# Kernel tuning notes

Hardware: AMD Instinct MI355X
Metric: run time of the kernel (lower is better)

The kernel has to match this reference:

```python
import jax, jax.numpy as jnp
import numpy as np

B, N, K = 2, 8192, 9
IN_CH, FEAT_CH, COST_CH = 64, 128, 64

def _bn(x, p, eps=1e-5):
    # eval-mode BatchNorm; p is [4, C] = (gamma, beta, running_mean, running_var)
    sh = (1, -1) + (1,) * (x.ndim - 2)
    g, b, m, v = (p[i].reshape(sh) for i in range(4))
    return (x - m) / jnp.sqrt(v + eps) * g + b

def _c1(x, w, b):
    # Conv1d kernel 1: x [B,C,N], w [O,C]
    return jnp.einsum('oc,bcn->bon', w, x) + b[None, :, None]

def _forward(xyz, points, cost_volume, feats, flow,
             w0, b0, bn0, w1, b1, bn1,
             wz, bz, wr, br, wq, bq,
             w2a, b2a, w2b, b2b, wfc, bfc,
             rw0, rbn0, rw1, rbn1, rw2, rbn2,
             cw0, cbn0, cw1, cbn1, cw2, cbn2):
    lrelu = lambda t: jax.nn.leaky_relu(t, 0.1)
    # --- self-KNN on xyz ---
    xt = jnp.transpose(xyz, (0, 2, 1))                   # B N 3
    sq = jnp.sum(xt * xt, -1)                            # B N
    d2 = sq[:, :, None] + sq[:, None, :] - 2.0 * jnp.einsum('bnd,bmd->bnm', xt, xt)
    idx = jax.lax.top_k(-d2, K)[1]                       # B N K (nearest incl. self)
    # --- grouping_operation: gather neighbor features ---
    np0 = jnp.concatenate([cost_volume, flow], 1)        # B (cost_ch+3) N
    g = jax.vmap(lambda p, i: p[:, i])(np0, idx)         # B C N K
    # --- Conv2d(1x1)+BN+LeakyReLU stack ---
    g = lrelu(_bn(jnp.einsum('oc,bcnk->bonk', w0, g) + b0[None, :, None, None], bn0))
    g = lrelu(_bn(jnp.einsum('oc,bcnk->bonk', w1, g) + b1[None, :, None, None], bn1))
    h = jnp.max(g, -1)                                   # max over neighbors -> B 128 N
    # --- ConvGRU(x=feats, h) with 1x1 Conv1d gates ---
    hx = jnp.concatenate([h, feats], 1)
    z = jax.nn.sigmoid(_c1(hx, wz, bz))
    r = jax.nn.sigmoid(_c1(hx, wr, br))
    q = jnp.tanh(_c1(jnp.concatenate([r * h, feats], 1), wq, bq))
    h = (1.0 - z) * h + z * q
    # --- Conv1d MLP head ---
    x = jnp.concatenate([points, h], 1)                  # B (in_ch+128) N
    x = lrelu(_c1(x, w2a, b2a))
    x = lrelu(_c1(x, w2b, b2b))
    re_flow = _c1(x, wfc, bfc)                           # B 3 N
    # --- prob regnets (Conv1d no-bias + BN + ReLU) ---
    def reg(y, ws, ps):
        for w, p in zip(ws, ps):
            y = jax.nn.relu(_bn(jnp.einsum('oc,bcn->bon', w, y), p))
        return y
    refine = reg(x, [rw0, rw1, rw2], [rbn0, rbn1, rbn2])         # B 1 N
    coarse = reg(cost_volume, [cw0, cw1, cw2], [cbn0, cbn1, cbn2])
    re_flow = coarse * flow + refine * re_flow
    return x, jnp.clip(re_flow, -20.0, 20.0)

def setup_inputs():
    key = jax.random.key(0)
    ks = iter(jax.random.split(key, 80))
    nrm = lambda shape, s=1.0: jax.random.normal(next(ks), shape, jnp.float32) * s
    def bnp(C):
        g = jax.random.uniform(next(ks), (C,), jnp.float32) + 0.5
        b = nrm((C,), 0.1); m = nrm((C,), 0.1)
        v = jax.random.uniform(next(ks), (C,), jnp.float32) + 0.5
        return jnp.stack([g, b, m, v])
    z = lambda C: jnp.zeros((C,), jnp.float32)
    return dict(
        xyz=nrm((B, 3, N)), points=nrm((B, IN_CH, N)), cost_volume=nrm((B, COST_CH, N)),
        feats=nrm((B, FEAT_CH, N)), flow=nrm((B, 3, N), 0.1),
        w0=nrm((128, COST_CH + 3), 0.05), b0=z(128), bn0=bnp(128),
        w1=nrm((128, 128), 0.05), b1=z(128), bn1=bnp(128),
        wz=nrm((128, 256), 0.05), bz=z(128), wr=nrm((128, 256), 0.05), br=z(128),
        wq=nrm((128, 256), 0.05), bq=z(128),
        w2a=nrm((128, IN_CH + 128), 0.05), b2a=z(128), w2b=nrm((64, 128), 0.05), b2b=z(64),
        wfc=nrm((3, 64), 0.05), bfc=z(3),
        rw0=nrm((64, 64), 0.05), rbn0=bnp(64), rw1=nrm((64, 64), 0.05), rbn1=bnp(64),
        rw2=nrm((1, 64), 0.05), rbn2=bnp(1),
        cw0=nrm((64, COST_CH), 0.05), cbn0=bnp(64), cw1=nrm((64, 64), 0.05), cbn1=bnp(64),
        cw2=nrm((1, 64), 0.05), cbn2=bnp(1),
    )

def reference(xyz, points, cost_volume, feats, flow, w0, b0, bn0, w1, b1, bn1, wz, bz, wr, br, wq, bq, w2a, b2a, w2b, b2b, wfc, bfc, rw0, rbn0, rw1, rbn1, rw2, rbn2, cw0, cbn0, cw1, cbn1, cw2, cbn2):
    return _forward(xyz, points, cost_volume, feats, flow, w0, b0, bn0, w1, b1, bn1, wz, bz, wr, br, wq, bq, w2a, b2a, w2b, b2b, wfc, bfc, rw0, rbn0, rw1, rbn1, rw2, rbn2, cw0, cbn0, cw1, cbn1, cw2, cbn2)
```

## Files before the change

### kernel.cpp

```cpp
#include <hip/hip_runtime.h>
#include <math.h>

typedef __bf16 bf16;
typedef __bf16 bf16x8 __attribute__((ext_vector_type(8)));
typedef float f32x4 __attribute__((ext_vector_type(4)));

#define NPTS 8192
#define MTOT 16384

static __device__ __forceinline__ float b2f(bf16 x) { return (float)x; }
static __device__ __forceinline__ bf16  f2b(float x) { return (bf16)x; }

__global__ void diag_k(float* out, float code)
{
    if (threadIdx.x == 0 && blockIdx.x == 0) out[0] = code;
}

static __device__ __forceinline__ void pack_body(bf16 (*tile)[68],
                                                 const float* __restrict__ src, int Csrc,
                                                 bf16* __restrict__ dst, int ldd,
                                                 int nb, int cb, int b)
{
    const int t = threadIdx.x;
#pragma unroll
    for (int i = 0; i < 8; ++i) {
        int id = t + i * 256;
        int c = id >> 6, n = id & 63;
        int cc = cb + c;
        bf16 v = (bf16)0.0f;
        if (cc < Csrc) v = f2b(src[(size_t)(b * Csrc + cc) * NPTS + nb + n]);
        tile[c][n] = v;
    }
    __syncthreads();
#pragma unroll
    for (int i = 0; i < 8; ++i) {
        int id = t + i * 256;
        int n = id >> 5, c = id & 31;
        dst[(size_t)(b * NPTS + nb + n) * ldd + cb + c] = tile[c][n];
    }
}

static __device__ __forceinline__ float tau_decode(unsigned long long k8)
{
    unsigned u = (unsigned)(k8 >> 32);
    unsigned m = 0x80000000u | (unsigned)(~((int)u >> 31));
    return __uint_as_float(u ^ m);
}

static __device__ __forceinline__ void mm32(
    f32x4 (&acc)[2][2],
    const bf16* A1, int lda1, int row01, int K1,
    const bf16* A2, int lda2, int row02,
    const bf16* W, int ldw, int K, int ob)
{
    const int lane = threadIdx.x & 63;
    const int q = lane >> 4, r = lane & 15;
    const bf16* Wp = W + (size_t)(ob + r) * ldw + q * 8;
    for (int k = 0; k < K; k += 32) {
        const bf16* Ap; int ld;
        if (k < K1) { ld = lda1; Ap = A1 + (size_t)(row01 + r) * lda1 + q * 8 + k; }
        else        { ld = lda2; Ap = A2 + (size_t)(row02 + r) * lda2 + q * 8 + (k - K1); }
        bf16x8 bv0 = *(const bf16x8*)(Wp + k);
        bf16x8 bv1 = *(const bf16x8*)(Wp + 16 * ldw + k);
        bf16x8 a0 = *(const bf16x8*)(Ap);
        bf16x8 a1 = *(const bf16x8*)(Ap + 16 * ld);
        acc[0][0] = __builtin_amdgcn_mfma_f32_16x16x32_bf16(a0, bv0, acc[0][0], 0, 0, 0);
        acc[1][0] = __builtin_amdgcn_mfma_f32_16x16x32_bf16(a1, bv0, acc[1][0], 0, 0, 0);
        acc[0][1] = __builtin_amdgcn_mfma_f32_16x16x32_bf16(a0, bv1, acc[0][1], 0, 0, 0);
        acc[1][1] = __builtin_amdgcn_mfma_f32_16x16x32_bf16(a1, bv1, acc[1][1], 0, 0, 0);
    }
}

static __device__ __forceinline__ void zacc(f32x4 (&acc)[2][2])
{
    f32x4 z = {0.f, 0.f, 0.f, 0.f};
    acc[0][0] = z; acc[0][1] = z; acc[1][0] = z; acc[1][1] = z;
}

__global__ __launch_bounds__(256) void pack_a(
    const float* __restrict__ w0, const float* __restrict__ w1,
    const float* __restrict__ wz, const float* __restrict__ wr,
    const float* __restrict__ wq, const float* __restrict__ w2a,
    const float* __restrict__ w2b, const float* __restrict__ rw0,
    const float* __restrict__ rw1, const float* __restrict__ cw0,
    const float* __restrict__ cw1,
    const float* __restrict__ cost, const float* __restrict__ flow,
    bf16* __restrict__ w0p, bf16* __restrict__ wts,
    bf16* __restrict__ CV, bf16* __restrict__ FL)
{
    __shared__ __align__(16) bf16 tile[32][68];
    const int bx = blockIdx.x;
    if (bx < 48) {
        int id = bx * 256 + threadIdx.x;
        if (id < 128 * 96) {
            int o = id / 96, c = id - o * 96;
            w0p[id] = (c < 67) ? f2b(w0[o * 67 + c]) : (bf16)0.0f;
        }
    } else if (bx < 688) {
        int id = (bx - 48) * 256 + threadIdx.x;
        if (id < 163840) {
            const float* s; int off;
            if (id < 16384)       { s = w1;  off = 0; }
            else if (id < 49152)  { s = wz;  off = 16384; }
            else if (id < 81920)  { s = wr;  off = 49152; }
            else if (id < 114688) { s = wq;  off = 81920; }
            else if (id < 139264) { s = w2a; off = 114688; }
            else if (id < 147456) { s = w2b; off = 139264; }
            else if (id < 151552) { s = rw0; off = 147456; }
            else if (id < 155648) { s = rw1; off = 151552; }
            else if (id < 159744) { s = cw0; off = 155648; }
            else                  { s = cw1; off = 159744; }
            wts[id] = f2b(s[id - off]);
        }
    } else if (bx < 1200) {
        int l = bx - 688, x = l & 127, r2 = l >> 7;
        pack_body(tile, cost, 64, CV, 64, x * 64, (r2 & 1) * 32, r2 >> 1);
    } else {
        int l = bx - 1200, x = l & 127, b = l >> 7;
        pack_body(tile, flow, 3, FL, 32, x * 64, 0, b);
    }
}

__global__ __launch_bounds__(256, 5) void knn_conv_packb(
    const float* __restrict__ xyz, const float* __restrict__ feats,
    const float* __restrict__ points,
    const bf16* __restrict__ CV, const bf16* __restrict__ FL,
    const bf16* __restrict__ W0p, const bf16* __restrict__ W1,
    const float* __restrict__ b0, const float* __restrict__ bn0,
    const float* __restrict__ b1, const float* __restrict__ bn1,
    bf16* __restrict__ FE, bf16* __restrict__ PT,
    bf16* __restrict__ P2, int* __restrict__ idxg)
{
    __shared__ __align__(16) char smem[16384];
    const int bx = blockIdx.x;
    if (bx < 4096) {
        float4* pts = (float4*)smem;
        const int t = threadIdx.x, lane = t & 63, w = t >> 6;
        const int qid = bx * 4 + w, b = qid >> 13;
        const float* X = xyz + b * 3 * NPTS;
        const int n = qid & (NPTS - 1);
        const float qx = X[n], qy = X[NPTS + n], qz = X[2 * NPTS + n];
        const float qsq = qx * qx + qy * qy + qz * qz;

        unsigned long long kk[9];
#pragma unroll
        for (int k = 0; k < 9; ++k) kk[k] = ~0ull;
        float tau = __builtin_inff();

        for (int ch = 0; ch < 8; ++ch) {
            __syncthreads();
#pragma unroll
            for (int r2 = 0; r2 < 4; ++r2) {
                int i2 = t + r2 * 256;
                int ci = ch * 1024 + i2;
                float x = X[ci], y = X[NPTS + ci], z = X[2 * NPTS + ci];
                pts[i2] = make_float4(x, y, z, x * x + y * y + z * z);
            }
            __syncthreads();
            int i0 = 0;
            if (ch == 0) {
                float4 c = pts[lane];
                float d = (qsq + c.w) - 2.0f * (qx * c.x + qy * c.y + qz * c.z);
                unsigned kd = __float_as_uint(d);
                kd ^= ((unsigned)((int)kd >> 31)) | 0x80000000u;
                unsigned long long key = ((unsigned long long)kd << 32) | (unsigned)lane;
#pragma unroll
                for (int r = 0; r < 9; ++r) {
                    unsigned long long m = key;
#pragma unroll
                    for (int s = 1; s < 64; s <<= 1) {
                        unsigned long long o = __shfl_xor(m, s);
                        if (o < m) m = o;
                    }
                    kk[r] = m;
                    if (key == m) key = ~0ull;
                }
                tau = tau_decode(kk[8]);
                i0 = 1;
            }
            for (int i = i0; i < 16; ++i) {
                float4 c = pts[i * 64 + lane];
                float d = (qsq + c.w) - 2.0f * (qx * c.x + qy * c.y + qz * c.z);
                unsigned long long mask = __ballot(d <= tau);
                if (mask) {
                    const int base = ch * 1024 + i * 64;
                    do {
                        int L = __builtin_ctzll(mask);
                        mask &= mask - 1;
                        float dL = __uint_as_float(
                            (unsigned)__builtin_amdgcn_readlane(__float_as_int(d), L));
                        unsigned kd = __float_as_uint(dL);
                        kd ^= ((unsigned)((int)kd >> 31)) | 0x80000000u;
                        unsigned long long K = ((unsigned long long)kd << 32)
                                             | (unsigned)(base + L);
                        if (K < kk[8]) {
                            bool lt[9];
#pragma unroll
                            for (int j2 = 0; j2 < 9; ++j2) lt[j2] = K < kk[j2];
#pragma unroll
                            for (int j2 = 8; j2 > 0; --j2)
                                kk[j2] = lt[j2] ? (lt[j2 - 1] ? kk[j2 - 1] : K) : kk[j2];
                            kk[0] = lt[0] ? K : kk[0];
                            tau = tau_decode(kk[8]);
                        }
                    } while (mask);
                }
            }
        }
        if (lane == 0) {
#pragma unroll
            for (int k = 0; k < 9; ++k) {
                int m = (int)(unsigned)(kk[k] & 0xffffffffu);
                m = ((unsigned)m < (unsigned)NPTS) ? m : 0;
                idxg[qid * 9 + k] = b * NPTS + m;
            }
        }
    } else if (bx < 4608) {
        bf16 (*P1t)[136] = (bf16 (*)[136])smem;
        const int w = threadIdx.x >> 6, lane = threadIdx.x & 63;
        const int q = lane >> 4, r = lane & 15;
        const int ptb = (bx - 4096) * 32;
        {
            f32x4 acc[2][2]; zacc(acc);
            const int ob = w * 32;
            mm32(acc, CV, 64, ptb, 64, FL, 32, ptb, W0p, 96, 96, ob);
#pragma unroll
            for (int to = 0; to < 2; ++to) {
                const int o = ob + to * 16 + r;
                float bs = b0[o];
                float gg = bn0[o], be = bn0[128 + o], mm = bn0[256 + o];
                float rs = 1.0f / sqrtf(bn0[384 + o] + 1e-5f);
#pragma unroll
                for (int tm = 0; tm < 2; ++tm) {
#pragma unroll
                    for (int rr = 0; rr < 4; ++rr) {
                        const int jl = tm * 16 + q * 4 + rr;
                        float v = acc[tm][to][rr] + bs;
                        v = (v - mm) * rs * gg + be;
                        v = v > 0.f ? v : 0.1f * v;
                        P1t[jl][o] = f2b(v);
                    }
                }
            }
        }
        __syncthreads();
        {
            f32x4 acc[2][2]; zacc(acc);
            const int ob = w * 32;
            mm32(acc, &P1t[0][0], 136, 0, 128, &P1t[0][0], 136, 0, W1, 128, 128, ob);
#pragma unroll
            for (int to = 0; to < 2; ++to) {
                const int o = ob + to * 16 + r;
                float bs = b1[o];
                float gg = bn1[o], be = bn1[128 + o], mm = bn1[256 + o];
                float rs = 1.0f / sqrtf(bn1[384 + o] + 1e-5f);
#pragma unroll
                for (int tm = 0; tm < 2; ++tm) {
#pragma unroll
                    for (int rr = 0; rr < 4; ++rr) {
                        const int jl = tm * 16 + q * 4 + rr;
                        float v = acc[tm][to][rr] + bs;
                        v = (v - mm) * rs * gg + be;
                        v = v > 0.f ? v : 0.1f * v;
                        P2[(size_t)(ptb + jl) * 128 + o] = f2b(v);
                    }
                }
            }
        }
    } else if (bx < 5632) {
        bf16 (*tile)[68] = (bf16 (*)[68])smem;
        int l = bx - 4608, x = l & 127, r2 = l >> 7;
        pack_body(tile, feats, 128, FE, 128, x * 64, (r2 & 3) * 32, r2 >> 2);
    } else {
        bf16 (*tile)[68] = (bf16 (*)[68])smem;
        int l = bx - 5632, x = l & 127, r2 = l >> 7;
        pack_body(tile, points, 64, PT, 64, x * 64, (r2 & 1) * 32, r2 >> 1);
    }
}

struct MRP {
    const bf16 *P2, *FE, *PT, *CV;
    const int  *idx;
    const bf16 *WZ, *WR, *WQ, *W2A, *W2B, *RW0, *RW1, *CW0, *CW1;
    const float *bz, *br, *bq, *b2a, *b2b;
    const float *rbn0, *rbn1, *cbn0, *cbn1;
    const float *rw2, *rbn2, *cw2, *cbn2, *wfc, *bfc, *flow;
    float* out;
};

__global__ __launch_bounds__(256) void megarow(MRP p)
{
    __shared__ __align__(16) bf16 Zt[32][136], RHt[32][136], HPt[32][136], X1t[32][136];
    __shared__ __align__(16) bf16 X2t[32][72], R1t[32][72], R2t[32][72],
                                  C1t[32][72], C2t[32][72];
    __shared__ int idxt[32][9];
    const int w = threadIdx.x >> 6, lane = threadIdx.x & 63;
    const int q = lane >> 4, r = lane & 15;
    const int ptb = blockIdx.x * 32;

    for (int id = threadIdx.x; id < 288; id += 256) {
        int jl = id / 9, k = id - jl * 9;
        int m = p.idx[(ptb + jl) * 9 + k];
        idxt[jl][k] = ((unsigned)m < (unsigned)MTOT) ? m : 0;
    }
    __syncthreads();
    {
        const int o = threadIdx.x & 127;
        const int j0 = (threadIdx.x >> 7) * 16;
#pragma unroll 4
        for (int i = 0; i < 16; ++i) {
            const int jl = j0 + i;
            float v = -__builtin_inff();
#pragma unroll
            for (int k = 0; k < 9; ++k)
                v = fmaxf(v, b2f(p.P2[(size_t)idxt[jl][k] * 128 + o]));
            X1t[jl][o] = f2b(v);
        }
    }
    __syncthreads();

    {
        const int ob = w * 32;
        f32x4 acc[2][2]; zacc(acc);
        mm32(acc, &X1t[0][0], 136, 0, 128, p.FE, 128, ptb, p.WZ, 256, 256, ob);
#pragma unroll
        for (int to = 0; to < 2; ++to) {
            const int o = ob + to * 16 + r;
            const float bs = p.bz[o];
#pragma unroll
            for (int tm = 0; tm < 2; ++tm)
#pragma unroll
                for (int rr = 0; rr < 4; ++rr) {
                    const int jl = tm * 16 + q * 4 + rr;
                    float v = acc[tm][to][rr] + bs;
                    Zt[jl][o] = f2b(1.0f / (1.0f + expf(-v)));
                }
        }
        f32x4 acc2[2][2]; zacc(acc2);
        mm32(acc2, &X1t[0][0], 136, 0, 128, p.FE, 128, ptb, p.WR, 256, 256, ob);
#pragma unroll
        for (int to = 0; to < 2; ++to) {
            const int o = ob + to * 16 + r;
            const float bs = p.br[o];
#pragma unroll
            for (int tm = 0; tm < 2; ++tm)
#pragma unroll
                for (int rr = 0; rr < 4; ++rr) {
                    const int jl = tm * 16 + q * 4 + rr;
                    float v = acc2[tm][to][rr] + bs;
                    v = 1.0f / (1.0f + expf(-v));
                    RHt[jl][o] = f2b(v * b2f(X1t[jl][o]));
                }
        }
    }
    __syncthreads();
    {
        const int ob = w * 32;
        f32x4 acc[2][2]; zacc(acc);
        mm32(acc, &RHt[0][0], 136, 0, 128, p.FE, 128, ptb, p.WQ, 256, 256, ob);
#pragma unroll
        for (int to = 0; to < 2; ++to) {
            const int o = ob + to * 16 + r;
            const float bs = p.bq[o];
#pragma unroll
            for (int tm = 0; tm < 2; ++tm)
#pragma unroll
                for (int rr = 0; rr < 4; ++rr) {
                    const int jl = tm * 16 + q * 4 + rr;
                    float v = acc[tm][to][rr] + bs;
                    float qv = tanhf(v);
                    float z = b2f(Zt[jl][o]);
                    float h = b2f(X1t[jl][o]);
                    HPt[jl][o] = f2b((1.0f - z) * h + z * qv);
                }
        }
    }
    __syncthreads();
    {
        const int ob = w * 32;
        f32x4 acc[2][2]; zacc(acc);
        mm32(acc, p.PT, 64, ptb, 64, &HPt[0][0], 136, 0, p.W2A, 192, 192, ob);
#pragma unroll
        for (int to = 0; to < 2; ++to) {
            const int o = ob + to * 16 + r;
            const float bs = p.b2a[o];
#pragma unroll
            for (int tm = 0; tm < 2; ++tm)
#pragma unroll
                for (int rr = 0; rr < 4; ++rr) {
                    const int jl = tm * 16 + q * 4 + rr;
                    float v = acc[tm][to][rr] + bs;
                    X1t[jl][o] = f2b(v > 0.f ? v : 0.1f * v);
                }
        }
    }
    __syncthreads();
    if (w < 2) {
        const int ob = w * 32;
        f32x4 acc[2][2]; zacc(acc);
        mm32(acc, &X1t[0][0], 136, 0, 128, &X1t[0][0], 136, 0, p.W2B, 128, 128, ob);
#pragma unroll
        for (int to = 0; to < 2; ++to) {
            const int o = ob + to * 16 + r;
            const float bs = p.b2b[o];
#pragma unroll
            for (int tm = 0; tm < 2; ++tm)
#pragma unroll
                for (int rr = 0; rr < 4; ++rr) {
                    const int jl = tm * 16 + q * 4 + rr;
                    float v = acc[tm][to][rr] + bs;
                    v = v > 0.f ? v : 0.1f * v;
                    X2t[jl][o] = f2b(v);
                    const int j = ptb + jl, bb = j >> 13, nn = j & (NPTS - 1);
                    p.out[(size_t)bb * 64 * NPTS + (size_t)o * NPTS + nn] = v;
                }
        }
    } else {
        const int ob = (w - 2) * 32;
        f32x4 acc[2][2]; zacc(acc);
        mm32(acc, p.CV, 64, ptb, 64, p.CV, 64, ptb, p.CW0, 64, 64, ob);
#pragma unroll
        for (int to = 0; to < 2; ++to) {
            const int o = ob + to * 16 + r;
            float gg = p.cbn0[o], be = p.cbn0[64 + o], mm = p.cbn0[128 + o];
            float rs = 1.0f / sqrtf(p.cbn0[192 + o] + 1e-5f);
#pragma unroll
            for (int tm = 0; tm < 2; ++tm)
#pragma unroll
                for (int rr = 0; rr < 4; ++rr) {
                    const int jl = tm * 16 + q * 4 + rr;
                    float v = acc[tm][to][rr];
                    v = (v - mm) * rs * gg + be;
                    C1t[jl][o] = f2b(fmaxf(v, 0.f));
                }
        }
    }
    __syncthreads();
    if (w < 2) {
        const int ob = w * 32;
        f32x4 acc[2][2]; zacc(acc);
        mm32(acc, &X2t[0][0], 72, 0, 64, &X2t[0][0], 72, 0, p.RW0, 64, 64, ob);
#pragma unroll
        for (int to = 0; to < 2; ++to) {
            const int o = ob + to * 16 + r;
            float gg = p.rbn0[o], be = p.rbn0[64 + o], mm = p.rbn0[128 + o];
            float rs = 1.0f / sqrtf(p.rbn0[192 + o] + 1e-5f);
#pragma unroll
            for (int tm = 0; tm < 2; ++tm)
#pragma unroll
                for (int rr = 0; rr < 4; ++rr) {
                    const int jl = tm * 16 + q * 4 + rr;
                    float v = acc[tm][to][rr];
                    v = (v - mm) * rs * gg + be;
                    R1t[jl][o] = f2b(fmaxf(v, 0.f));
                }
        }
    } else {
        const int ob = (w - 2) * 32;
        f32x4 acc[2][2]; zacc(acc);
        mm32(acc, &C1t[0][0], 72, 0, 64, &C1t[0][0], 72, 0, p.CW1, 64, 64, ob);
#pragma unroll
        for (int to = 0; to < 2; ++to) {
            const int o = ob + to * 16 + r;
            float gg = p.cbn1[o], be = p.cbn1[64 + o], mm = p.cbn1[128 + o];
            float rs = 1.0f / sqrtf(p.cbn1[192 + o] + 1e-5f);
#pragma unroll
            for (int tm = 0; tm < 2; ++tm)
#pragma unroll
                for (int rr = 0; rr < 4; ++rr) {
                    const int jl = tm * 16 + q * 4 + rr;
                    float v = acc[tm][to][rr];
                    v = (v - mm) * rs * gg + be;
                    C2t[jl][o] = f2b(fmaxf(v, 0.f));
                }
        }
    }
    __syncthreads();
    if (w < 2) {
        const int ob = w * 32;
        f32x4 acc[2][2]; zacc(acc);
        mm32(acc, &R1t[0][0], 72, 0, 64, &R1t[0][0], 72, 0, p.RW1, 64, 64, ob);
#pragma unroll
        for (int to = 0; to < 2; ++to) {
            const int o = ob + to * 16 + r;
            float gg = p.rbn1[o], be = p.rbn1[64 + o], mm = p.rbn1[128 + o];
            float rs = 1.0f / sqrtf(p.rbn1[192 + o] + 1e-5f);
#pragma unroll
            for (int tm = 0; tm < 2; ++tm)
#pragma unroll
                for (int rr = 0; rr < 4; ++rr) {
                    const int jl = tm * 16 + q * 4 + rr;
                    float v = acc[tm][to][rr];
                    v = (v - mm) * rs * gg + be;
                    R2t[jl][o] = f2b(fmaxf(v, 0.f));
                }
        }
    }
    __syncthreads();
    if (threadIdx.x < 32) {
        const int jl = threadIdx.x, j = ptb + jl;
        const int b = j >> 13, n = j & (NPTS - 1);
        float dr = 0.f, dc = 0.f, p0 = 0.f, p1 = 0.f, p2 = 0.f;
#pragma unroll
        for (int c = 0; c < 64; ++c) {
            float x = b2f(X2t[jl][c]);
            dr += p.rw2[c] * b2f(R2t[jl][c]);
            dc += p.cw2[c] * b2f(C2t[jl][c]);
            p0 += p.wfc[c] * x;
            p1 += p.wfc[64 + c] * x;
            p2 += p.wfc[128 + c] * x;
        }
        float refine = (dr - p.rbn2[2]) / sqrtf(p.rbn2[3] + 1e-5f) * p.rbn2[0] + p.rbn2[1];
        refine = fmaxf(refine, 0.f);
        float coarse = (dc - p.cbn2[2]) / sqrtf(p.cbn2[3] + 1e-5f) * p.cbn2[0] + p.cbn2[1];
        coarse = fmaxf(coarse, 0.f);
        p0 += p.bfc[0]; p1 += p.bfc[1]; p2 += p.bfc[2];
        const float f0 = p.flow[(size_t)b * 3 * NPTS + n];
        const float f1 = p.flow[(size_t)b * 3 * NPTS + NPTS + n];
        const float f2v = p.flow[(size_t)b * 3 * NPTS + 2 * NPTS + n];
        float o0 = fminf(fmaxf(coarse * f0 + refine * p0, -20.f), 20.f);
        float o1 = fminf(fmaxf(coarse * f1 + refine * p1, -20.f), 20.f);
        float o2 = fminf(fmaxf(coarse * f2v + refine * p2, -20.f), 20.f);
        float* ro = p.out + 1048576;
        ro[(size_t)b * 3 * NPTS + n] = o0;
        ro[(size_t)b * 3 * NPTS + NPTS + n] = o1;
        ro[(size_t)b * 3 * NPTS + 2 * NPTS + n] = o2;
    }
}

extern "C" void kernel_launch(void* const* d_in, const int* in_sizes, int n_in,
                              void* d_out, int out_size, void* d_ws, size_t ws_size,
                              hipStream_t stream)
{
    static const int EXP[35] = {
        49152, 1048576, 1048576, 2097152, 49152,
        8576, 128, 512, 16384, 128, 512,
        32768, 128, 32768, 128, 32768, 128,
        24576, 128, 8192, 64, 192, 3,
        4096, 256, 4096, 256, 64, 4,
        4096, 256, 4096, 256, 64, 4 };
    float code = 0.f;
    if (n_in != 35) code = 900.f;
    else if (out_size != 1097728) code = 950.f;
    else if (ws_size < 18767872u) code = 980.f;
    else { for (int i = 0; i < 35; ++i) if (in_sizes[i] != EXP[i]) { code = 1000.f + 4.f * i; break; } }
    if (code != 0.f) { diag_k<<<dim3(1), dim3(64), 0, stream>>>((float*)d_out, code); return; }

    const float* xyz    = (const float*)d_in[0];
    const float* points = (const float*)d_in[1];
    const float* cost   = (const float*)d_in[2];
    const float* feats  = (const float*)d_in[3];
    const float* flow   = (const float*)d_in[4];
    const float* w0     = (const float*)d_in[5];
    const float* b0     = (const float*)d_in[6];
    const float* bn0    = (const float*)d_in[7];
    const float* w1     = (const float*)d_in[8];
    const float* b1     = (const float*)d_in[9];
    const float* bn1    = (const float*)d_in[10];
    const float* wz     = (const float*)d_in[11];
    const float* bz     = (const float*)d_in[12];
    const float* wr     = (const float*)d_in[13];
    const float* br     = (const float*)d_in[14];
    const float* wq     = (const float*)d_in[15];
    const float* bq     = (const float*)d_in[16];
    const float* w2a    = (const float*)d_in[17];
    const float* b2a    = (const float*)d_in[18];
    const float* w2b    = (const float*)d_in[19];
    const float* b2b    = (const float*)d_in[20];
    const float* wfc    = (const float*)d_in[21];
    const float* bfc    = (const float*)d_in[22];
    const float* rw0    = (const float*)d_in[23];
    const float* rbn0   = (const float*)d_in[24];
    const float* rw1    = (const float*)d_in[25];
    const float* rbn1   = (const float*)d_in[26];
    const float* rw2    = (const float*)d_in[27];
    const float* rbn2   = (const float*)d_in[28];
    const float* cw0    = (const float*)d_in[29];
    const float* cbn0   = (const float*)d_in[30];
    const float* cw1    = (const float*)d_in[31];
    const float* cbn1   = (const float*)d_in[32];
    const float* cw2    = (const float*)d_in[33];
    const float* cbn2   = (const float*)d_in[34];

    char* ws = (char*)d_ws;
    bf16* W0p  = (bf16*)(ws + 0);
    bf16* WTS  = (bf16*)(ws + 24576);
    int*  idxg = (int*) (ws + 352256);
    bf16* CV   = (bf16*)(ws + 942080);
    bf16* FL   = (bf16*)(ws + 3039232);
    bf16* FE   = (bf16*)(ws + 4087808);
    bf16* PT   = (bf16*)(ws + 8282112);
    bf16* P2   = (bf16*)(ws + 10379264);

    bf16* W1  = WTS;
    bf16* WZ  = WTS + 16384;
    bf16* WR  = WTS + 49152;
    bf16* WQ  = WTS + 81920;
    bf16* W2A = WTS + 114688;
    bf16* W2B = WTS + 139264;
    bf16* RW0 = WTS + 147456;
    bf16* RW1 = WTS + 151552;
    bf16* CW0 = WTS + 155648;
    bf16* CW1 = WTS + 159744;

    float* out = (float*)d_out;

     pack_a<<<dim3(1456), dim3(256), 0, stream>>>(
              w0, w1, wz, wr, wq, w2a, w2b, rw0, rw1, cw0, cw1,
              cost, flow, W0p, WTS, CV, FL);
     knn_conv_packb<<<dim3(6144), dim3(256), 0, stream>>>(
              xyz, feats, points, CV, FL, W0p, W1, b0, bn0, b1, bn1,
              FE, PT, P2, idxg);
     MRP mp;
          mp.P2 = P2; mp.FE = FE; mp.PT = PT; mp.CV = CV; mp.idx = idxg;
          mp.WZ = WZ; mp.WR = WR; mp.WQ = WQ; mp.W2A = W2A; mp.W2B = W2B;
          mp.RW0 = RW0; mp.RW1 = RW1; mp.CW0 = CW0; mp.CW1 = CW1;
          mp.bz = bz; mp.br = br; mp.bq = bq; mp.b2a = b2a; mp.b2b = b2b;
          mp.rbn0 = rbn0; mp.rbn1 = rbn1; mp.cbn0 = cbn0; mp.cbn1 = cbn1;
          mp.rw2 = rw2; mp.rbn2 = rbn2; mp.cw2 = cw2; mp.cbn2 = cbn2;
          mp.wfc = wfc; mp.bfc = bfc; mp.flow = flow; mp.out = out;
          megarow<<<dim3(512), dim3(256), 0, stream>>>(mp);

    (void)n_in;
}
```

Before: 281.7 us.

## Split KNN top-k keys into 32-bit arrays, vectorize gather-max, fuse Z/R GEMMs

The KNN insertion list now keeps 32-bit distance keys and indices in separate arrays instead of 64-bit packed keys, and the tau threshold is refreshed once per ballot batch rather than after every insert. The neighbour max-gather in megarow loads four bf16 channels per thread instead of one. The z and r gate GEMMs run in a single loop that shares the A-operand loads across both weight matrices. Tie-breaking on equal distances changes, since the index is no longer part of the comparison key, and the fused GEMM raises register pressure.

```diff
diff --git a/kernel.cpp b/kernel.cpp
--- a/kernel.cpp
+++ b/kernel.cpp
@@ -2,6 +2,7 @@
 #include <math.h>
 
 typedef __bf16 bf16;
+typedef __bf16 bf16x4 __attribute__((ext_vector_type(4)));
 typedef __bf16 bf16x8 __attribute__((ext_vector_type(8)));
 typedef float f32x4 __attribute__((ext_vector_type(4)));
 
@@ -40,9 +41,8 @@
     }
 }
 
-static __device__ __forceinline__ float tau_decode(unsigned long long k8)
-{
-    unsigned u = (unsigned)(k8 >> 32);
+static __device__ __forceinline__ float tau32(unsigned u)
+{
     unsigned m = 0x80000000u | (unsigned)(~((int)u >> 31));
     return __uint_as_float(u ^ m);
 }
@@ -71,6 +71,37 @@
     }
 }
 
+static __device__ __forceinline__ void mm32x2(
+    f32x4 (&acc)[2][2], f32x4 (&acc2)[2][2],
+    const bf16* A1, int lda1, int row01, int K1,
+    const bf16* A2, int lda2, int row02,
+    const bf16* Wa, const bf16* Wb, int ldw, int K, int ob)
+{
+    const int lane = threadIdx.x & 63;
+    const int q = lane >> 4, r = lane & 15;
+    const bf16* Wpa = Wa + (size_t)(ob + r) * ldw + q * 8;
+    const bf16* Wpb = Wb + (size_t)(ob + r) * ldw + q * 8;
+    for (int k = 0; k < K; k += 32) {
+        const bf16* Ap; int ld;
+        if (k < K1) { ld = lda1; Ap = A1 + (size_t)(row01 + r) * lda1 + q * 8 + k; }
+        else        { ld = lda2; Ap = A2 + (size_t)(row02 + r) * lda2 + q * 8 + (k - K1); }
+        bf16x8 a0 = *(const bf16x8*)(Ap);
+        bf16x8 a1 = *(const bf16x8*)(Ap + 16 * ld);
+        bf16x8 ba0 = *(const bf16x8*)(Wpa + k);
+        bf16x8 ba1 = *(const bf16x8*)(Wpa + 16 * ldw + k);
+        bf16x8 bb0 = *(const bf16x8*)(Wpb + k);
+        bf16x8 bb1 = *(const bf16x8*)(Wpb + 16 * ldw + k);
+        acc[0][0]  = __builtin_amdgcn_mfma_f32_16x16x32_bf16(a0, ba0, acc[0][0], 0, 0, 0);
+        acc[1][0]  = __builtin_amdgcn_mfma_f32_16x16x32_bf16(a1, ba0, acc[1][0], 0, 0, 0);
+        acc[0][1]  = __builtin_amdgcn_mfma_f32_16x16x32_bf16(a0, ba1, acc[0][1], 0, 0, 0);
+        acc[1][1]  = __builtin_amdgcn_mfma_f32_16x16x32_bf16(a1, ba1, acc[1][1], 0, 0, 0);
+        acc2[0][0] = __builtin_amdgcn_mfma_f32_16x16x32_bf16(a0, bb0, acc2[0][0], 0, 0, 0);
+        acc2[1][0] = __builtin_amdgcn_mfma_f32_16x16x32_bf16(a1, bb0, acc2[1][0], 0, 0, 0);
+        acc2[0][1] = __builtin_amdgcn_mfma_f32_16x16x32_bf16(a0, bb1, acc2[0][1], 0, 0, 0);
+        acc2[1][1] = __builtin_amdgcn_mfma_f32_16x16x32_bf16(a1, bb1, acc2[1][1], 0, 0, 0);
+    }
+}
+
 static __device__ __forceinline__ void zacc(f32x4 (&acc)[2][2])
 {
     f32x4 z = {0.f, 0.f, 0.f, 0.f};
@@ -142,9 +173,8 @@
         const float qx = X[n], qy = X[NPTS + n], qz = X[2 * NPTS + n];
         const float qsq = qx * qx + qy * qy + qz * qz;
 
-        unsigned long long kk[9];
-#pragma unroll
-        for (int k = 0; k < 9; ++k) kk[k] = ~0ull;
+        unsigned kd9[9];
+        int      id9[9];
         float tau = __builtin_inff();
 
         for (int ch = 0; ch < 8; ++ch) {
@@ -172,10 +202,11 @@
                         unsigned long long o = __shfl_xor(m, s);
                         if (o < m) m = o;
                     }
-                    kk[r] = m;
+                    kd9[r] = (unsigned)__builtin_amdgcn_readfirstlane((int)(m >> 32));
+                    id9[r] = __builtin_amdgcn_readfirstlane((int)(unsigned)(m & 0xffffffffu));
                     if (key == m) key = ~0ull;
                 }
-                tau = tau_decode(kk[8]);
+                tau = tau32(kd9[8]);
                 i0 = 1;
             }
             for (int i = i0; i < 16; ++i) {
@@ -187,30 +218,31 @@
                     do {
                         int L = __builtin_ctzll(mask);
                         mask &= mask - 1;
-                        float dL = __uint_as_float(
-                            (unsigned)__builtin_amdgcn_readlane(__float_as_int(d), L));
-                        unsigned kd = __float_as_uint(dL);
-                        kd ^= ((unsigned)((int)kd >> 31)) | 0x80000000u;
-                        unsigned long long K = ((unsigned long long)kd << 32)
-                                             | (unsigned)(base + L);
-                        if (K < kk[8]) {
+                        unsigned di = (unsigned)__builtin_amdgcn_readlane(
+                                          __float_as_int(d), L);
+                        unsigned kd = di ^ (((unsigned)((int)di >> 31)) | 0x80000000u);
+                        if (kd < kd9[8]) {
+                            const int idxn = base + L;
                             bool lt[9];
 #pragma unroll
-                            for (int j2 = 0; j2 < 9; ++j2) lt[j2] = K < kk[j2];
-#pragma unroll
-                            for (int j2 = 8; j2 > 0; --j2)
-                                kk[j2] = lt[j2] ? (lt[j2 - 1] ? kk[j2 - 1] : K) : kk[j2];
-                            kk[0] = lt[0] ? K : kk[0];
-                            tau = tau_decode(kk[8]);
+                            for (int j2 = 0; j2 < 9; ++j2) lt[j2] = kd < kd9[j2];
+#pragma unroll
+                            for (int j2 = 8; j2 > 0; --j2) {
+                                kd9[j2] = lt[j2] ? (lt[j2 - 1] ? kd9[j2 - 1] : kd) : kd9[j2];
+                                id9[j2] = lt[j2] ? (lt[j2 - 1] ? id9[j2 - 1] : idxn) : id9[j2];
+                            }
+                            kd9[0] = lt[0] ? kd : kd9[0];
+                            id9[0] = lt[0] ? idxn : id9[0];
                         }
                     } while (mask);
+                    tau = tau32(kd9[8]);
                 }
             }
         }
         if (lane == 0) {
 #pragma unroll
             for (int k = 0; k < 9; ++k) {
-                int m = (int)(unsigned)(kk[k] & 0xffffffffu);
+                int m = id9[k];
                 m = ((unsigned)m < (unsigned)NPTS) ? m : 0;
                 idxg[qid * 9 + k] = b * NPTS + m;
             }
@@ -305,24 +337,33 @@
     }
     __syncthreads();
     {
-        const int o = threadIdx.x & 127;
-        const int j0 = (threadIdx.x >> 7) * 16;
-#pragma unroll 4
-        for (int i = 0; i < 16; ++i) {
-            const int jl = j0 + i;
-            float v = -__builtin_inff();
-#pragma unroll
-            for (int k = 0; k < 9; ++k)
-                v = fmaxf(v, b2f(p.P2[(size_t)idxt[jl][k] * 128 + o]));
-            X1t[jl][o] = f2b(v);
+        const int c4 = (threadIdx.x & 31) * 4;
+        const int jr = threadIdx.x >> 5;
+#pragma unroll
+        for (int jj = 0; jj < 4; ++jj) {
+            const int jl = jr + 8 * jj;
+            float mx0 = -__builtin_inff(), mx1 = -__builtin_inff();
+            float mx2 = -__builtin_inff(), mx3 = -__builtin_inff();
+#pragma unroll
+            for (int k = 0; k < 9; ++k) {
+                bf16x4 v = *(const bf16x4*)(p.P2 + (size_t)idxt[jl][k] * 128 + c4);
+                mx0 = fmaxf(mx0, b2f(v[0]));
+                mx1 = fmaxf(mx1, b2f(v[1]));
+                mx2 = fmaxf(mx2, b2f(v[2]));
+                mx3 = fmaxf(mx3, b2f(v[3]));
+            }
+            bf16x4 st;
+            st[0] = f2b(mx0); st[1] = f2b(mx1); st[2] = f2b(mx2); st[3] = f2b(mx3);
+            *(bf16x4*)&X1t[jl][c4] = st;
         }
     }
     __syncthreads();
 
     {
         const int ob = w * 32;
-        f32x4 acc[2][2]; zacc(acc);
-        mm32(acc, &X1t[0][0], 136, 0, 128, p.FE, 128, ptb, p.WZ, 256, 256, ob);
+        f32x4 acc[2][2], acc2[2][2]; zacc(acc); zacc(acc2);
+        mm32x2(acc, acc2, &X1t[0][0], 136, 0, 128, p.FE, 128, ptb,
+               p.WZ, p.WR, 256, 256, ob);
 #pragma unroll
         for (int to = 0; to < 2; ++to) {
             const int o = ob + to * 16 + r;
@@ -336,8 +377,6 @@
                     Zt[jl][o] = f2b(1.0f / (1.0f + expf(-v)));
                 }
         }
-        f32x4 acc2[2][2]; zacc(acc2);
-        mm32(acc2, &X1t[0][0], 136, 0, 128, p.FE, 128, ptb, p.WR, 256, 256, ob);
 #pragma unroll
         for (int to = 0; to < 2; ++to) {
             const int o = ob + to * 16 + r;
```

Result: slower. 299.1 us (+6.2%).
